# Kernel tuning notes

Measured on AMD Instinct MI355X. Metric: run time of the kernel, lower is better.

## Reference

```python
import jax, jax.numpy as jnp
import numpy as np

N = 4096      # nodes
F = 128       # input feature dim
HEADS = 8     # attention_num
U = 8         # units per head


def setup_inputs() -> dict:
    key = jax.random.key(0)
    k_a, k_h, k_w, k_al, k_ar = jax.random.split(key, 5)
    A = jax.random.randint(k_a, (N, N), 0, 2).astype(jnp.float32)   # dense 0/1 adjacency
    H = jax.random.normal(k_h, (N, F), dtype=jnp.float32)
    W = jax.random.normal(k_w, (HEADS, F, U), dtype=jnp.float32) * 0.1
    a_left = jax.random.normal(k_al, (HEADS, U), dtype=jnp.float32) * 0.1
    a_right = jax.random.normal(k_ar, (HEADS, U), dtype=jnp.float32) * 0.1
    return {"A": A, "H": H, "W": W, "a_left": a_left, "a_right": a_right}


def reference(A, H, W, a_left, a_right):
    # Per-head attention logits: E[h,i,j] = e_left[h,i] + e_right[h,j]
    e_l = jnp.einsum('nf,hfu,hu->hn', H, W, a_left)    # [HEADS, N]
    e_r = jnp.einsum('nf,hfu,hu->hn', H, W, a_right)   # [HEADS, N]
    E = e_l[:, :, None] + e_r[:, None, :]              # [HEADS, N, N]
    # Faithful to original: denominator uses exp(E * A) (zeros in A -> exp(0)=1)
    denom = jnp.sum(jnp.exp(E * A[None]), axis=-1, keepdims=True)   # [HEADS, N, 1]
    Alpha = jnp.exp(E) / denom * A[None]               # masked attention weights
    # Aggregate then project: elu(Alpha @ H @ W) per head
    out = jax.nn.elu(jnp.einsum('hij,jf,hfu->hiu', Alpha, H, W))    # [HEADS, N, U]
    # is_output_layer=False -> concat heads along feature dim: [N, HEADS*U]
    return jnp.transpose(out, (1, 0, 2)).reshape(H.shape[0], HEADS * U)
```

## Files before the change

kernel.cpp:

```cpp
#include <hip/hip_runtime.h>
#include <hip/hip_bf16.h>

#define NN 4096
#define FF 128
#define NC 80

typedef __attribute__((ext_vector_type(4))) float float4v;
typedef __attribute__((ext_vector_type(4))) unsigned int uint4v;
typedef __attribute__((ext_vector_type(8))) short short8;

__global__ __launch_bounds__(256) void gat_prep(const float* __restrict__ H,
                                                const float* __restrict__ W,
                                                const float* __restrict__ al,
                                                const float* __restrict__ ar,
                                                float* __restrict__ expEl,
                                                __hip_bfloat16* __restrict__ Bp)
{
    __shared__ float Ws[FF * 64];
    __shared__ float Hs[16 * FF];
    const int t  = threadIdx.x;
    const int j0 = blockIdx.x * 16;

    #pragma unroll
    for (int i = 0; i < 32; ++i) {
        const int q = t + i * 256;
        const int f = q >> 6, hu = q & 63;
        Ws[q] = W[(size_t)(hu >> 3) * (FF * 8) + f * 8 + (hu & 7)];
    }
    #pragma unroll
    for (int i = 0; i < 8; ++i) {
        const int q = t + i * 256;
        Hs[q] = H[(size_t)j0 * FF + q];
    }
    __syncthreads();

    const int wave = t >> 6, lane = t & 63;
    const int h = lane >> 3, u = lane & 7;
    const float a_r = ar[lane], a_l = al[lane];

    #pragma unroll
    for (int jj = 0; jj < 4; ++jj) {
        const int jl = wave * 4 + jj;
        const int j  = j0 + jl;
        float acc = 0.f;
        #pragma unroll 8
        for (int f = 0; f < FF; ++f)
            acc += Hs[jl * FF + f] * Ws[f * 64 + lane];

        float vr = acc * a_r, vl = acc * a_l;
        #pragma unroll
        for (int s = 1; s < 8; s <<= 1) { vr += __shfl_xor(vr, s); vl += __shfl_xor(vl, s); }
        const float er = expf(vr);
        const float el = expf(vl);
        if (u == 0) expEl[h * NN + j] = el;
        const float er_b = __shfl(er, u * 8);

        const int kt = j >> 5, q = (j >> 3) & 3, j8 = j & 7;
        const size_t base = ((size_t)(kt * 4 + q) * NC) * 8 + j8;
        Bp[base + (size_t)lane * 8] = __float2bfloat16(er * acc);
        if (lane < 16) {
            const float v = (lane < 8) ? er_b : (lane == 8 ? 1.0f : 0.0f);
            Bp[base + (size_t)(64 + lane) * 8] = __float2bfloat16(v);
        }
    }
}

__global__ __launch_bounds__(256) void gat_gemm(const float* __restrict__ A,
                                                const __hip_bfloat16* __restrict__ Bp,
                                                float* __restrict__ Cp,
                                                int ktiles)
{
    const int rb   = blockIdx.x;
    const int kc   = blockIdx.y;
    const int wave = threadIdx.x >> 6;
    const int lane = threadIdx.x & 63;
    const int m16  = lane & 15;
    const int q    = lane >> 4;
    const int row0 = rb * 64 + wave * 16;

    float4v acc[5] = {};

    const int k0 = kc * (ktiles * 32);
    const unsigned int* Au = (const unsigned int*)A;
    const short* Bs = (const short*)Bp;
    const unsigned int* arow = Au + (size_t)(row0 + m16) * NN + q * 8;

    uint4v a0 = *(const uint4v*)(arow + k0);
    uint4v a1 = *(const uint4v*)(arow + k0 + 4);

    for (int kt = 0; kt < ktiles; ++kt) {
        const int kk = k0 + kt * 32;
        short8 afrag;
        afrag[0] = (short)(a0[0] >> 16); afrag[1] = (short)(a0[1] >> 16);
        afrag[2] = (short)(a0[2] >> 16); afrag[3] = (short)(a0[3] >> 16);
        afrag[4] = (short)(a1[0] >> 16); afrag[5] = (short)(a1[1] >> 16);
        afrag[6] = (short)(a1[2] >> 16); afrag[7] = (short)(a1[3] >> 16);

        if (kt + 1 < ktiles) {
            a0 = *(const uint4v*)(arow + kk + 32);
            a1 = *(const uint4v*)(arow + kk + 36);
        }

        const int ktg = kk >> 5;
        const short8* bbase = (const short8*)(Bs + ((size_t)(ktg * 4 + q) * NC) * 8);
        #pragma unroll
        for (int nt = 0; nt < 5; ++nt) {
            short8 bfrag = bbase[nt * 16 + m16];
            acc[nt] = __builtin_amdgcn_mfma_f32_16x16x32_bf16(afrag, bfrag, acc[nt], 0, 0, 0);
        }
    }

    float* cbase = Cp + (size_t)kc * NN * NC;
    #pragma unroll
    for (int nt = 0; nt < 5; ++nt) {
        #pragma unroll
        for (int r = 0; r < 4; ++r) {
            const int row = row0 + q * 4 + r;
            const int col = nt * 16 + m16;
            cbase[(size_t)row * NC + col] = acc[nt][r];
        }
    }
}

__global__ __launch_bounds__(256) void gat_epilogue(const float* __restrict__ Cp,
                                                    const float* __restrict__ expEl,
                                                    float* __restrict__ out,
                                                    int KC)
{
    const int idx = blockIdx.x * 256 + threadIdx.x;
    const int i = idx >> 6;
    const int c = idx & 63;
    const int h = c >> 3;

    float T = 0.f, S = 0.f, dg = 0.f;
    for (int kc = 0; kc < KC; ++kc) {
        const float* row = Cp + ((size_t)kc * NN + i) * NC;
        T  += row[c];
        S  += row[64 + h];
        dg += row[72];
    }
    const float el = expEl[h * NN + i];
    const float denom = ((float)NN - dg) + el * S;
    const float x = el * T / denom;
    const float y = x > 0.f ? x : expf(x) - 1.f;
    out[idx] = y;
}

extern "C" void kernel_launch(void* const* d_in, const int* in_sizes, int n_in,
                              void* d_out, int out_size, void* d_ws, size_t ws_size,
                              hipStream_t stream) {
    const float* A  = (const float*)d_in[0];
    const float* H  = (const float*)d_in[1];
    const float* W  = (const float*)d_in[2];
    const float* al = (const float*)d_in[3];
    const float* ar = (const float*)d_in[4];
    float* out = (float*)d_out;

    float* expEl = (float*)d_ws;
    __hip_bfloat16* Bp = (__hip_bfloat16*)((char*)d_ws + 131072);
    float* Cp = (float*)((char*)d_ws + 131072 + 655360);

    const size_t fixed = 131072 + 655360;
    int KC = 16;
    while (KC > 1 && fixed + (size_t)KC * NN * NC * 4 > ws_size) KC >>= 1;
    const int ktiles = NN / (KC * 32);

    gat_prep<<<NN / 16, 256, 0, stream>>>(H, W, al, ar, expEl, Bp);
    gat_gemm<<<dim3(NN / 64, KC), 256, 0, stream>>>(A, Bp, Cp, ktiles);
    gat_epilogue<<<NN * 64 / 256, 256, 0, stream>>>(Cp, expEl, out, KC);
}
```

Before: 125.4 us.

## Compute H·W projection on MFMA with split-bf16 and fold attention vectors into W

The prep kernel's scalar FP32 H·W dot products are replaced with bf16 MFMA using a hi/lo split (three MFMAs per tile) to keep near-FP32 accuracy. The attention vectors a_left and a_right are folded into extra W columns, so the logits come straight out of the GEMM instead of from shuffle reductions. Blocks now cover 32 nodes with 128 threads. Separately, the K-split count of the main GEMM drops from 16 to 8, halving partial-sum traffic in the epilogue at the cost of fewer GEMM blocks.

```diff
diff --git a/kernel.cpp b/kernel.cpp
--- a/kernel.cpp
+++ b/kernel.cpp
@@ -4,64 +4,136 @@
 #define NN 4096
 #define FF 128
 #define NC 80
+#define HPAD 136
 
 typedef __attribute__((ext_vector_type(4))) float float4v;
 typedef __attribute__((ext_vector_type(4))) unsigned int uint4v;
 typedef __attribute__((ext_vector_type(8))) short short8;
-
-__global__ __launch_bounds__(256) void gat_prep(const float* __restrict__ H,
+typedef __attribute__((ext_vector_type(8))) unsigned short ushort8;
+typedef __attribute__((ext_vector_type(4))) unsigned short ushort4v;
+
+static __device__ inline unsigned short bfb(float x) {
+    __hip_bfloat16 b = __float2bfloat16(x);
+    return *(unsigned short*)&b;
+}
+static __device__ inline float bff(unsigned short u) {
+    __hip_bfloat16 b = *(__hip_bfloat16*)&u;
+    return __bfloat162float(b);
+}
+
+__global__ __launch_bounds__(128) void gat_prep(const float* __restrict__ H,
                                                 const float* __restrict__ W,
                                                 const float* __restrict__ al,
                                                 const float* __restrict__ ar,
                                                 float* __restrict__ expEl,
                                                 __hip_bfloat16* __restrict__ Bp)
 {
-    __shared__ float Ws[FF * 64];
-    __shared__ float Hs[16 * FF];
+    __shared__ unsigned short Hhi[32 * HPAD], Hlo[32 * HPAD];
+    __shared__ unsigned short Whi[16 * NC * 8], Wlo[16 * NC * 8];
     const int t  = threadIdx.x;
-    const int j0 = blockIdx.x * 16;
-
-    #pragma unroll
-    for (int i = 0; i < 32; ++i) {
-        const int q = t + i * 256;
-        const int f = q >> 6, hu = q & 63;
-        Ws[q] = W[(size_t)(hu >> 3) * (FF * 8) + f * 8 + (hu & 7)];
-    }
-    #pragma unroll
-    for (int i = 0; i < 8; ++i) {
-        const int q = t + i * 256;
-        Hs[q] = H[(size_t)j0 * FF + q];
+    const int j0 = blockIdx.x * 32;
+
+    {
+        const int jr = t >> 2, f0 = (t & 3) * 32;
+        const float* src = H + (size_t)(j0 + jr) * FF + f0;
+        unsigned short* dh = Hhi + jr * HPAD + f0;
+        unsigned short* dl = Hlo + jr * HPAD + f0;
+        #pragma unroll
+        for (int i = 0; i < 32; i += 4) {
+            float4v x = *(const float4v*)(src + i);
+            ushort4v hv, lv;
+            #pragma unroll
+            for (int c2 = 0; c2 < 4; ++c2) {
+                unsigned short h = bfb(x[c2]);
+                hv[c2] = h;
+                lv[c2] = bfb(x[c2] - bff(h));
+            }
+            *(ushort4v*)(dh + i) = hv;
+            *(ushort4v*)(dl + i) = lv;
+        }
+    }
+    {
+        const int hu = t & 63;
+        const int fb = (t >> 6) * 64;
+        const float* wsrc = W + (size_t)(hu >> 3) * (FF * 8) + (hu & 7);
+        #pragma unroll
+        for (int g8 = 0; g8 < 8; ++g8) {
+            const int f0 = fb + g8 * 8;
+            ushort8 hv, lv;
+            #pragma unroll
+            for (int i = 0; i < 8; ++i) {
+                float x = wsrc[(size_t)(f0 + i) * 8];
+                unsigned short h = bfb(x);
+                hv[i] = h; lv[i] = bfb(x - bff(h));
+            }
+            const int g = (f0 >> 5) * 4 + ((f0 >> 3) & 3);
+            *(ushort8*)&Whi[((size_t)g * NC + hu) * 8] = hv;
+            *(ushort8*)&Wlo[((size_t)g * NC + hu) * 8] = lv;
+        }
+    }
+    {
+        const int h  = t >> 4;
+        const int f0 = (t & 15) * 8;
+        float arv[8], alv[8];
+        #pragma unroll
+        for (int u = 0; u < 8; ++u) { arv[u] = ar[h * 8 + u]; alv[u] = al[h * 8 + u]; }
+        ushort8 rh, rl, lh, ll;
+        #pragma unroll
+        for (int i = 0; i < 8; ++i) {
+            const float* wp = W + (size_t)h * (FF * 8) + (size_t)(f0 + i) * 8;
+            float sr = 0.f, sl = 0.f;
+            #pragma unroll
+            for (int u = 0; u < 8; ++u) { float w = wp[u]; sr += w * arv[u]; sl += w * alv[u]; }
+            unsigned short a = bfb(sr); rh[i] = a; rl[i] = bfb(sr - bff(a));
+            unsigned short b = bfb(sl); lh[i] = b; ll[i] = bfb(sl - bff(b));
+        }
+        const int g = (f0 >> 5) * 4 + ((f0 >> 3) & 3);
+        *(ushort8*)&Whi[((size_t)g * NC + 64 + h) * 8] = rh;
+        *(ushort8*)&Wlo[((size_t)g * NC + 64 + h) * 8] = rl;
+        *(ushort8*)&Whi[((size_t)g * NC + 72 + h) * 8] = lh;
+        *(ushort8*)&Wlo[((size_t)g * NC + 72 + h) * 8] = ll;
     }
     __syncthreads();
 
-    const int wave = t >> 6, lane = t & 63;
-    const int h = lane >> 3, u = lane & 7;
-    const float a_r = ar[lane], a_l = al[lane];
-
-    #pragma unroll
-    for (int jj = 0; jj < 4; ++jj) {
-        const int jl = wave * 4 + jj;
-        const int j  = j0 + jl;
-        float acc = 0.f;
-        #pragma unroll 8
-        for (int f = 0; f < FF; ++f)
-            acc += Hs[jl * FF + f] * Ws[f * 64 + lane];
-
-        float vr = acc * a_r, vl = acc * a_l;
-        #pragma unroll
-        for (int s = 1; s < 8; s <<= 1) { vr += __shfl_xor(vr, s); vl += __shfl_xor(vl, s); }
-        const float er = expf(vr);
-        const float el = expf(vl);
-        if (u == 0) expEl[h * NN + j] = el;
-        const float er_b = __shfl(er, u * 8);
-
-        const int kt = j >> 5, q = (j >> 3) & 3, j8 = j & 7;
-        const size_t base = ((size_t)(kt * 4 + q) * NC) * 8 + j8;
-        Bp[base + (size_t)lane * 8] = __float2bfloat16(er * acc);
-        if (lane < 16) {
-            const float v = (lane < 8) ? er_b : (lane == 8 ? 1.0f : 0.0f);
-            Bp[base + (size_t)(64 + lane) * 8] = __float2bfloat16(v);
-        }
+    const int w = t >> 6, lane = t & 63;
+    const int m16 = lane & 15, q = lane >> 4;
+
+    float4v acc[5] = {};
+    #pragma unroll
+    for (int kt = 0; kt < 4; ++kt) {
+        short8 ahi = *(const short8*)&Hhi[(w * 16 + m16) * HPAD + kt * 32 + q * 8];
+        short8 alo = *(const short8*)&Hlo[(w * 16 + m16) * HPAD + kt * 32 + q * 8];
+        #pragma unroll
+        for (int nt = 0; nt < 5; ++nt) {
+            short8 bhi = *(const short8*)&Whi[((size_t)(kt * 4 + q) * NC + nt * 16 + m16) * 8];
+            short8 blo = *(const short8*)&Wlo[((size_t)(kt * 4 + q) * NC + nt * 16 + m16) * 8];
+            acc[nt] = __builtin_amdgcn_mfma_f32_16x16x32_bf16(ahi, bhi, acc[nt], 0, 0, 0);
+            acc[nt] = __builtin_amdgcn_mfma_f32_16x16x32_bf16(alo, bhi, acc[nt], 0, 0, 0);
+            acc[nt] = __builtin_amdgcn_mfma_f32_16x16x32_bf16(ahi, blo, acc[nt], 0, 0, 0);
+        }
+    }
+
+    const int jbase = j0 + w * 16 + q * 4;
+    float ex[4];
+    #pragma unroll
+    for (int r = 0; r < 4; ++r) ex[r] = expf(acc[4][r]);
+    if (m16 >= 8) {
+        #pragma unroll
+        for (int r = 0; r < 4; ++r)
+            expEl[(m16 - 8) * NN + jbase + r] = ex[r];
+    }
+    #pragma unroll
+    for (int r = 0; r < 4; ++r) {
+        const int j = jbase + r;
+        const size_t base = ((size_t)((j >> 5) * 4 + ((j >> 3) & 3)) * NC) * 8 + (j & 7);
+        #pragma unroll
+        for (int nt = 0; nt < 4; ++nt) {
+            const int srcl = (lane & 48) | (nt * 2 + (m16 >> 3));
+            const float er = __shfl(ex[r], srcl);
+            Bp[base + (size_t)(nt * 16 + m16) * 8] = __float2bfloat16(er * acc[nt][r]);
+        }
+        const float v = (m16 < 8) ? ex[r] : (m16 == 8 ? 1.0f : 0.0f);
+        Bp[base + (size_t)(64 + m16) * 8] = __float2bfloat16(v);
     }
 }
 
@@ -161,11 +233,11 @@
     float* Cp = (float*)((char*)d_ws + 131072 + 655360);
 
     const size_t fixed = 131072 + 655360;
-    int KC = 16;
+    int KC = 8;
     while (KC > 1 && fixed + (size_t)KC * NN * NC * 4 > ws_size) KC >>= 1;
     const int ktiles = NN / (KC * 32);
 
-    gat_prep<<<NN / 16, 256, 0, stream>>>(H, W, al, ar, expEl, Bp);
+    gat_prep<<<NN / 32, 128, 0, stream>>>(H, W, al, ar, expEl, Bp);
     gat_gemm<<<dim3(NN / 64, KC), 256, 0, stream>>>(A, Bp, Cp, ktiles);
     gat_epilogue<<<NN * 64 / 256, 256, 0, stream>>>(Cp, expEl, out, KC);
 }
```

Measured after the change: 122.3 us. 2.5% less time.
